# Performance work log

Measured on AMD Instinct MI355X. Metric: run time of the kernel, lower is better.

Reference implementation:

```python
import jax, jax.numpy as jnp
import numpy as np

B, S, D = 2, 2048, 1024
H = 16
HD = D // H  # 64
EPS = 1e-5
ROPE_BASE = 10000.0


def _rope_cos_sin(seq_len, head_dim, dtype):
    # inv_freq over even channel indices, standard rotate-half RoPE
    inv_freq = 1.0 / (ROPE_BASE ** (jnp.arange(0, head_dim, 2, dtype=jnp.float32) / head_dim))
    ang = jnp.arange(seq_len, dtype=jnp.float32)[:, None] * inv_freq[None, :]  # [S, HD/2]
    emb = jnp.concatenate([ang, ang], axis=-1)  # [S, HD]
    return jnp.cos(emb).astype(dtype), jnp.sin(emb).astype(dtype)


def _rotate_half(x):
    x1, x2 = jnp.split(x, 2, axis=-1)
    return jnp.concatenate([-x2, x1], axis=-1)


def setup_inputs() -> dict:
    key = jax.random.key(0)
    ks = jax.random.split(key, 5)
    std = 0.023  # default init_method: normal(mean=0, std=0.023)
    return {
        "hidden_states": jax.random.normal(ks[0], (B, S, D), dtype=jnp.float32),
        "ln_gamma": jnp.ones((D,), dtype=jnp.float32),
        "ln_beta": jnp.zeros((D,), dtype=jnp.float32),
        "qkv_weight": jax.random.normal(ks[1], (3 * D, D), dtype=jnp.float32) * std,
        "qkv_bias": jax.random.normal(ks[2], (3 * D,), dtype=jnp.float32) * std,
        "proj_weight": jax.random.normal(ks[3], (D, D), dtype=jnp.float32) * std,
        "proj_bias": jax.random.normal(ks[4], (D,), dtype=jnp.float32) * std,
    }


def reference(hidden_states, ln_gamma, ln_beta, qkv_weight, qkv_bias, proj_weight, proj_bias):
    b, s, d = hidden_states.shape
    # --- input LayerNorm ---
    mu = jnp.mean(hidden_states, axis=-1, keepdims=True)
    var = jnp.mean(jnp.square(hidden_states - mu), axis=-1, keepdims=True)
    x = (hidden_states - mu) * jax.lax.rsqrt(var + EPS) * ln_gamma + ln_beta

    # --- fused QKV projection (interleaved per-head q,k,v) ---
    qkv = x @ qkv_weight.T + qkv_bias  # [B,S,3D]
    qkv = qkv.reshape(b, s, H, 3, HD)
    q, k, v = qkv[..., 0, :], qkv[..., 1, :], qkv[..., 2, :]  # each [B,S,H,HD]

    # --- RoPE on q and k ---
    cos, sin = _rope_cos_sin(s, HD, q.dtype)  # [S,HD]
    cos = cos[None, :, None, :]
    sin = sin[None, :, None, :]
    q = q * cos + _rotate_half(q) * sin
    k = k * cos + _rotate_half(k) * sin

    # --- causal scaled-dot-product attention ---
    scale = 1.0 / jnp.sqrt(jnp.asarray(HD, dtype=q.dtype))
    scores = jnp.einsum("bqhd,bkhd->bhqk", q, k) * scale  # [B,H,S,S]
    causal = jnp.tril(jnp.ones((s, s), dtype=bool))
    scores = jnp.where(causal[None, None, :, :], scores, jnp.finfo(scores.dtype).min)
    probs = jax.nn.softmax(scores, axis=-1)
    ctx = jnp.einsum("bhqk,bkhd->bqhd", probs, v).reshape(b, s, d)

    # --- output projection ---
    return ctx @ proj_weight.T + proj_bias
```

## Files before the change

kernel.cpp:

```cpp
#include <hip/hip_runtime.h>
#include <math.h>

#define B_  2
#define S_  2048
#define D_  1024
#define H_  16
#define HD_ 64
#define BS_ (B_ * S_)

typedef __bf16 bf16_t;
typedef __bf16 bf16x8 __attribute__((ext_vector_type(8)));
typedef __bf16 bf16x4 __attribute__((ext_vector_type(4)));
typedef float  f32x4  __attribute__((ext_vector_type(4)));
typedef short  s16x4  __attribute__((ext_vector_type(4)));

#define QSCALE 0.18033688011112042f
#define FREQC  0.28782313662425575f

__device__ __forceinline__ void async_ld16(const bf16_t* g, bf16_t* l)
{
    __builtin_amdgcn_global_load_lds(
        (const __attribute__((address_space(1))) void*)g,
        (__attribute__((address_space(3))) void*)l,
        16, 0, 0);
}

__global__ __launch_bounds__(256) void cvt_w(const float* __restrict__ a,
                                             const float* __restrict__ b,
                                             bf16_t* __restrict__ oa,
                                             bf16_t* __restrict__ ob)
{
    int idx = blockIdx.x * 256 + threadIdx.x;
    const int NA = 3 * D_ * D_ / 4;
    if (idx < NA) {
        float4 v = ((const float4*)a)[idx];
        bf16x4 p;
        p[0] = (bf16_t)v.x; p[1] = (bf16_t)v.y; p[2] = (bf16_t)v.z; p[3] = (bf16_t)v.w;
        ((bf16x4*)oa)[idx] = p;
    } else {
        int j = idx - NA;
        float4 v = ((const float4*)b)[j];
        bf16x4 p;
        p[0] = (bf16_t)v.x; p[1] = (bf16_t)v.y; p[2] = (bf16_t)v.z; p[3] = (bf16_t)v.w;
        ((bf16x4*)ob)[j] = p;
    }
}

__global__ __launch_bounds__(256) void ln_kernel(const float* __restrict__ x,
                                                 const float* __restrict__ gamma,
                                                 const float* __restrict__ beta,
                                                 bf16_t* __restrict__ y)
{
    int row = blockIdx.x;
    float4 v = ((const float4*)(x + (size_t)row * D_))[threadIdx.x];
    float sum = v.x + v.y + v.z + v.w;
    float sq  = v.x * v.x + v.y * v.y + v.z * v.z + v.w * v.w;
#pragma unroll
    for (int off = 32; off > 0; off >>= 1) {
        sum += __shfl_down(sum, off);
        sq  += __shfl_down(sq, off);
    }
    __shared__ float s_sum[4], s_sq[4];
    int wave = threadIdx.x >> 6;
    if ((threadIdx.x & 63) == 0) { s_sum[wave] = sum; s_sq[wave] = sq; }
    __syncthreads();
    float tsum = s_sum[0] + s_sum[1] + s_sum[2] + s_sum[3];
    float tsq  = s_sq[0] + s_sq[1] + s_sq[2] + s_sq[3];
    float mean = tsum * (1.0f / D_);
    float var  = tsq * (1.0f / D_) - mean * mean;
    float rstd = rsqrtf(var + 1e-5f);
    float4 g = ((const float4*)gamma)[threadIdx.x];
    float4 b = ((const float4*)beta)[threadIdx.x];
    bf16x4 o;
    o[0] = (bf16_t)((v.x - mean) * rstd * g.x + b.x);
    o[1] = (bf16_t)((v.y - mean) * rstd * g.y + b.y);
    o[2] = (bf16_t)((v.z - mean) * rstd * g.z + b.z);
    o[3] = (bf16_t)((v.w - mean) * rstd * g.w + b.w);
    *(bf16x4*)&y[(size_t)row * D_ + threadIdx.x * 4] = o;
}

template<int MODE>
__global__ __launch_bounds__(256) void gemm_bf16(const bf16_t* __restrict__ A,
                                                 const bf16_t* __restrict__ W,
                                                 const float* __restrict__ bias,
                                                 float* __restrict__ outf,
                                                 bf16_t* __restrict__ qout,
                                                 bf16_t* __restrict__ kout,
                                                 bf16_t* __restrict__ vout,
                                                 int M, int N, int K)
{
    constexpr int SMEM = (MODE == 1) ? 18432 : 16384;
    __shared__ bf16_t smem[SMEM];
    const int bm = blockIdx.y * 128, bn = blockIdx.x * 128;
    const int tid = threadIdx.x;
    const int wave = tid >> 6, lane = tid & 63;
    const int ln16 = lane & 15, quad = lane >> 4;
    const int wr = (wave >> 1) * 64, wc = (wave & 1) * 64;
    const int slot_a = (quad ^ (ln16 & 3)) * 8;

    f32x4 acc[4][4];
#pragma unroll
    for (int i = 0; i < 4; i++)
#pragma unroll
        for (int j = 0; j < 4; j++) acc[i][j] = (f32x4){0.f, 0.f, 0.f, 0.f};

#pragma unroll
    for (int j = 0; j < 2; j++) {
        int e = j * 256 + tid;
        int r = e >> 2, cg = ((e & 3) ^ (r & 3)) * 8;
        async_ld16(&A[(size_t)(bm + r) * K + cg], smem + e * 8);
        async_ld16(&W[(size_t)(bn + r) * K + cg], smem + 4096 + e * 8);
    }
    __syncthreads();

    for (int k0 = 0, it = 0; k0 < K; k0 += 32, it++) {
        const bf16_t* cur = smem + (it & 1) * 8192;
        bf16_t* nxt = smem + ((it & 1) ^ 1) * 8192;
        if (k0 + 32 < K) {
#pragma unroll
            for (int j = 0; j < 2; j++) {
                int e = j * 256 + tid;
                int r = e >> 2, cg = ((e & 3) ^ (r & 3)) * 8;
                async_ld16(&A[(size_t)(bm + r) * K + k0 + 32 + cg], nxt + e * 8);
                async_ld16(&W[(size_t)(bn + r) * K + k0 + 32 + cg], nxt + 4096 + e * 8);
            }
        }

        bf16x8 af[4], bf[4];
#pragma unroll
        for (int mi = 0; mi < 4; mi++)
            af[mi] = *(const bf16x8*)&cur[(wr + mi * 16 + ln16) * 32 + slot_a];
#pragma unroll
        for (int ni = 0; ni < 4; ni++)
            bf[ni] = *(const bf16x8*)&cur[4096 + (wc + ni * 16 + ln16) * 32 + slot_a];
#pragma unroll
        for (int mi = 0; mi < 4; mi++)
#pragma unroll
            for (int ni = 0; ni < 4; ni++)
                acc[mi][ni] = __builtin_amdgcn_mfma_f32_16x16x32_bf16(
                    af[mi], bf[ni], acc[mi][ni], 0, 0, 0);

        __syncthreads();
    }

#pragma unroll
    for (int ni = 0; ni < 4; ni++) {
        float bb = bias[bn + wc + ni * 16 + ln16];
#pragma unroll
        for (int mi = 0; mi < 4; mi++)
#pragma unroll
            for (int r = 0; r < 4; r++) acc[mi][ni][r] += bb;
    }

    if (MODE == 0) {
#pragma unroll
        for (int ni = 0; ni < 4; ni++) {
            int n = bn + wc + ni * 16 + ln16;
#pragma unroll
            for (int mi = 0; mi < 4; mi++)
#pragma unroll
                for (int r = 0; r < 4; r++)
                    outf[(size_t)(bm + wr + mi * 16 + quad * 4 + r) * N + n] = acc[mi][ni][r];
        }
    } else {
        const int n64 = (bn + wc) >> 6;
        const int t = n64 % 3, h = n64 / 3;
        bf16_t* T = smem + wave * (64 * 72);
        if (t == 2) {
#pragma unroll
            for (int mi = 0; mi < 4; mi++) {
#pragma unroll
                for (int ni = 0; ni < 4; ni++) {
                    bf16x4 pk;
#pragma unroll
                    for (int r = 0; r < 4; r++) pk[r] = (bf16_t)acc[mi][ni][r];
                    *(bf16x4*)&T[(ni * 16 + ln16) * 72 + mi * 16 + quad * 4] = pk;
                }
            }
            int m0 = bm + wr;
            int bi = m0 >> 11, s0g = m0 & (S_ - 1);
#pragma unroll
            for (int e = lane; e < 512; e += 64) {
                int hd_l = e >> 3, c8 = (e & 7) << 3;
                *(bf16x8*)&vout[((size_t)(bi * H_ + h) * HD_ + hd_l) * S_ + s0g + c8] =
                    *(const bf16x8*)&T[hd_l * 72 + c8];
            }
        } else {
            float fr0 = __expf(-(float)ln16 * FREQC);
            float fr1 = __expf(-(float)(16 + ln16) * FREQC);
            float sc = (t == 0) ? QSCALE : 1.0f;
#pragma unroll
            for (int mi = 0; mi < 4; mi++) {
#pragma unroll
                for (int r = 0; r < 4; r++) {
                    int m = bm + wr + mi * 16 + quad * 4 + r;
                    float s = (float)(m & (S_ - 1));
                    float sn0, cs0, sn1, cs1;
                    __sincosf(s * fr0, &sn0, &cs0);
                    __sincosf(s * fr1, &sn1, &cs1);
                    int rowo = (mi * 16 + quad * 4 + r) * 72;
                    float x1 = acc[mi][0][r], x2 = acc[mi][2][r];
                    T[rowo + ln16]      = (bf16_t)((x1 * cs0 - x2 * sn0) * sc);
                    T[rowo + 32 + ln16] = (bf16_t)((x2 * cs0 + x1 * sn0) * sc);
                    x1 = acc[mi][1][r]; x2 = acc[mi][3][r];
                    T[rowo + 16 + ln16] = (bf16_t)((x1 * cs1 - x2 * sn1) * sc);
                    T[rowo + 48 + ln16] = (bf16_t)((x2 * cs1 + x1 * sn1) * sc);
                }
            }
            bf16_t* dst = (t == 0) ? qout : kout;
#pragma unroll
            for (int e = lane; e < 512; e += 64) {
                int row_l = e >> 3, c8 = (e & 7) << 3;
                int m = bm + wr + row_l;
                int b = m >> 11, s = m & (S_ - 1);
                *(bf16x8*)&dst[((size_t)(b * H_ + h) * S_ + s) * HD_ + c8] =
                    *(const bf16x8*)&T[row_l * 72 + c8];
            }
        }
    }
}

__global__ __launch_bounds__(256) void attn_p1(const bf16_t* __restrict__ q_buf,
                                               const bf16_t* __restrict__ k_buf,
                                               const bf16_t* __restrict__ v_t,
                                               bf16_t* __restrict__ part_o,
                                               float* __restrict__ part_ml)
{
    __shared__ bf16_t KS[2][4096];
    __shared__ bf16_t VS[2][4096];

    const int x = blockIdx.x, h = blockIdx.y, b = blockIdx.z;
    const int t = (x < 32) ? (31 - x) : (x - 16);
    const int c = (x < 32) ? 0 : 1;
    const int k0c = c * 16;
    const int k1c = min(t, k0c + 15);

    const int tid = threadIdx.x;
    const int wave = tid >> 6, lane = tid & 63;
    const int ln16 = lane & 15, quad = lane >> 4;
    const int w0 = t * 64 + wave * 16;
    const int s7 = ln16 & 7;

    const bf16_t* qb = q_buf + (size_t)(b * H_ + h) * S_ * HD_;
    const bf16_t* kb = k_buf + (size_t)(b * H_ + h) * S_ * HD_;
    const bf16_t* vb = v_t  + (size_t)(b * H_ + h) * HD_ * S_;

    const int e0 = tid, e1 = tid + 256;
    const int r0 = e0 >> 3, c0 = ((e0 & 7) ^ (r0 & 7)) * 8;
    const int r1 = e1 >> 3, c1 = ((e1 & 7) ^ (r1 & 7)) * 8;

    bf16x8 qf[2];
#pragma unroll
    for (int kc = 0; kc < 2; kc++)
        qf[kc] = *(const bf16x8*)&qb[(size_t)(w0 + ln16) * HD_ + kc * 32 + quad * 8];

    f32x4 o[4];
#pragma unroll
    for (int mi = 0; mi < 4; mi++) o[mi] = (f32x4){0.f, 0.f, 0.f, 0.f};
    float m_i = -1e30f, l_i = 0.f;

    {
        bf16x8 ka = *(const bf16x8*)&kb[(size_t)(k0c * 64 + r0) * HD_ + c0];
        bf16x8 kc_ = *(const bf16x8*)&kb[(size_t)(k0c * 64 + r1) * HD_ + c1];
        bf16x8 va = *(const bf16x8*)&vb[(size_t)r0 * S_ + k0c * 64 + c0];
        bf16x8 vc = *(const bf16x8*)&vb[(size_t)r1 * S_ + k0c * 64 + c1];
        int b0 = k0c & 1;
        *(bf16x8*)&KS[b0][e0 * 8] = ka;
        *(bf16x8*)&KS[b0][e1 * 8] = kc_;
        *(bf16x8*)&VS[b0][e0 * 8] = va;
        *(bf16x8*)&VS[b0][e1 * 8] = vc;
    }
    int tp = (k0c + 1 <= k1c) ? (k0c + 1) : k1c;
    bf16x8 kp0 = *(const bf16x8*)&kb[(size_t)(tp * 64 + r0) * HD_ + c0];
    bf16x8 kp1 = *(const bf16x8*)&kb[(size_t)(tp * 64 + r1) * HD_ + c1];
    bf16x8 vp0 = *(const bf16x8*)&vb[(size_t)r0 * S_ + tp * 64 + c0];
    bf16x8 vp1 = *(const bf16x8*)&vb[(size_t)r1 * S_ + tp * 64 + c1];
    __syncthreads();

    for (int kt = k0c; kt <= k1c; kt++) {
        int tn = (kt + 2 <= k1c) ? (kt + 2) : k1c;
        bf16x8 kn0 = *(const bf16x8*)&kb[(size_t)(tn * 64 + r0) * HD_ + c0];
        bf16x8 kn1 = *(const bf16x8*)&kb[(size_t)(tn * 64 + r1) * HD_ + c1];
        bf16x8 vn0 = *(const bf16x8*)&vb[(size_t)r0 * S_ + tn * 64 + c0];
        bf16x8 vn1 = *(const bf16x8*)&vb[(size_t)r1 * S_ + tn * 64 + c1];

        int nb = (kt + 1) & 1;
        *(bf16x8*)&KS[nb][e0 * 8] = kp0;
        *(bf16x8*)&KS[nb][e1 * 8] = kp1;
        *(bf16x8*)&VS[nb][e0 * 8] = vp0;
        *(bf16x8*)&VS[nb][e1 * 8] = vp1;

        const bf16_t* Kc = &KS[kt & 1][0];
        const bf16_t* Vc = &VS[kt & 1][0];

        f32x4 st[4];
#pragma unroll
        for (int cb = 0; cb < 4; cb++) st[cb] = (f32x4){0.f, 0.f, 0.f, 0.f};
#pragma unroll
        for (int kc = 0; kc < 2; kc++)
#pragma unroll
            for (int cb = 0; cb < 4; cb++) {
                bf16x8 kf = *(const bf16x8*)&Kc[(cb * 16 + ln16) * 64 + ((kc * 4 + quad) ^ s7) * 8];
                st[cb] = __builtin_amdgcn_mfma_f32_16x16x32_bf16(kf, qf[kc], st[cb], 0, 0, 0);
            }

        if (kt == t) {
            int q_g = w0 + ln16;
#pragma unroll
            for (int cb = 0; cb < 4; cb++) {
                int key0 = kt * 64 + cb * 16 + quad * 4;
#pragma unroll
                for (int r = 0; r < 4; r++)
                    if (key0 + r > q_g) st[cb][r] = -1e30f;
            }
        }

        float mx = st[0][0];
#pragma unroll
        for (int cb = 0; cb < 4; cb++)
#pragma unroll
            for (int r = 0; r < 4; r++) mx = fmaxf(mx, st[cb][r]);
        mx = fmaxf(mx, __shfl_xor(mx, 16));
        mx = fmaxf(mx, __shfl_xor(mx, 32));
        float mn = fmaxf(m_i, mx);
        float sum = 0.f;
#pragma unroll
        for (int cb = 0; cb < 4; cb++)
#pragma unroll
            for (int r = 0; r < 4; r++) {
                float p = exp2f(st[cb][r] - mn);
                st[cb][r] = p;
                sum += p;
            }
        sum += __shfl_xor(sum, 16);
        sum += __shfl_xor(sum, 32);
        float al = exp2f(m_i - mn);
        l_i = l_i * al + sum;
        m_i = mn;
#pragma unroll
        for (int mi = 0; mi < 4; mi++) {
            o[mi][0] *= al; o[mi][1] *= al; o[mi][2] *= al; o[mi][3] *= al;
        }

        s16x4 pf4[4];
#pragma unroll
        for (int cb = 0; cb < 4; cb++) {
            union { bf16x4 hv; s16x4 sv; } u;
#pragma unroll
            for (int r = 0; r < 4; r++) u.hv[r] = (bf16_t)st[cb][r];
            pf4[cb] = u.sv;
        }

#pragma unroll
        for (int cb = 0; cb < 4; cb++) {
            int slot = ((cb * 2 + (quad >> 1)) ^ s7) * 8 + (quad & 1) * 4;
#pragma unroll
            for (int mi = 0; mi < 4; mi++) {
                union { bf16x4 hv; s16x4 sv; } uv;
                uv.hv = *(const bf16x4*)&Vc[(mi * 16 + ln16) * 64 + slot];
                o[mi] = __builtin_amdgcn_mfma_f32_16x16x16bf16_1k(uv.sv, pf4[cb], o[mi], 0, 0, 0);
            }
        }

        kp0 = kn0; kp1 = kn1; vp0 = vn0; vp1 = vn1;

        __syncthreads();
    }

    const size_t pidx = (((size_t)(b * H_ + h) * 32) + t) * 2 + c;
    bf16_t* po = part_o + pidx * 4096;
    const int q_l = wave * 16 + ln16;
#pragma unroll
    for (int mi = 0; mi < 4; mi++) {
        bf16x4 pk;
#pragma unroll
        for (int r = 0; r < 4; r++) pk[r] = (bf16_t)o[mi][r];
        *(bf16x4*)&po[q_l * 64 + mi * 16 + quad * 4] = pk;
    }
    if (quad == 0) {
        part_ml[pidx * 128 + q_l]      = m_i;
        part_ml[pidx * 128 + 64 + q_l] = l_i;
    }
}

__global__ __launch_bounds__(256) void attn_p2(const bf16_t* __restrict__ part_o,
                                               const float* __restrict__ part_ml,
                                               bf16_t* __restrict__ ctx)
{
    const int t = blockIdx.x, h = blockIdx.y, b = blockIdx.z;
    const int nch = (t >> 4) + 1;
    const size_t pidx = (((size_t)(b * H_ + h) * 32) + t) * 2;
    const int q_l = threadIdx.x >> 2;
    const int hg = (threadIdx.x & 3) * 16;

    float m0 = part_ml[pidx * 128 + q_l];
    float l0 = part_ml[pidx * 128 + 64 + q_l];
    const bf16_t* o0 = part_o + pidx * 4096 + q_l * 64 + hg;

    float w0, w1 = 0.f;
    const bf16_t* o1 = o0;
    if (nch == 2) {
        float m1 = part_ml[(pidx + 1) * 128 + q_l];
        float l1 = part_ml[(pidx + 1) * 128 + 64 + q_l];
        float M = fmaxf(m0, m1);
        float a0 = exp2f(m0 - M), a1 = exp2f(m1 - M);
        float L = a0 * l0 + a1 * l1;
        w0 = a0 / L; w1 = a1 / L;
        o1 = part_o + (pidx + 1) * 4096 + q_l * 64 + hg;
    } else {
        w0 = 1.f / l0;
    }

    bf16x8 a0v = *(const bf16x8*)o0;
    bf16x8 a1v = *(const bf16x8*)(o0 + 8);
    bf16x8 b0v = *(const bf16x8*)o1;
    bf16x8 b1v = *(const bf16x8*)(o1 + 8);
    bf16x8 out0, out1;
#pragma unroll
    for (int i = 0; i < 8; i++) {
        float f0 = (float)a0v[i] * w0 + (float)b0v[i] * w1;
        float f1 = (float)a1v[i] * w0 + (float)b1v[i] * w1;
        out0[i] = (bf16_t)f0;
        out1[i] = (bf16_t)f1;
    }
    bf16_t* dst = &ctx[(size_t)(b * S_ + t * 64 + q_l) * D_ + h * HD_ + hg];
    *(bf16x8*)dst = out0;
    *(bf16x8*)(dst + 8) = out1;
}

extern "C" void kernel_launch(void* const* d_in, const int* in_sizes, int n_in,
                              void* d_out, int out_size, void* d_ws, size_t ws_size,
                              hipStream_t stream)
{
    const float* hidden = (const float*)d_in[0];
    const float* gamma  = (const float*)d_in[1];
    const float* beta   = (const float*)d_in[2];
    const float* qkv_w  = (const float*)d_in[3];
    const float* qkv_b  = (const float*)d_in[4];
    const float* proj_w = (const float*)d_in[5];
    const float* proj_b = (const float*)d_in[6];
    float* out = (float*)d_out;

    char* ws = (char*)d_ws;
    const size_t MB = 1024 * 1024;
    bf16_t* x_ln = (bf16_t*)(ws);
    bf16_t* wq   = (bf16_t*)(ws +  8 * MB);
    bf16_t* wp   = (bf16_t*)(ws + 14 * MB);
    bf16_t* qbf  = (bf16_t*)(ws + 16 * MB);
    bf16_t* kbf  = (bf16_t*)(ws + 24 * MB);
    bf16_t* vtb  = (bf16_t*)(ws + 32 * MB);
    bf16_t* ctx  = (bf16_t*)(ws + 40 * MB);
    bf16_t* po   = (bf16_t*)(ws + 48 * MB);
    float*  pml  = (float*)(ws + 64 * MB);

    cvt_w<<<4096, 256, 0, stream>>>(qkv_w, proj_w, wq, wp);
    ln_kernel<<<BS_, 256, 0, stream>>>(hidden, gamma, beta, x_ln);
    gemm_bf16<1><<<dim3(24, 32), 256, 0, stream>>>(
        x_ln, wq, qkv_b, nullptr, qbf, kbf, vtb, BS_, 3 * D_, D_);
    attn_p1<<<dim3(48, H_, B_), 256, 0, stream>>>(qbf, kbf, vtb, po, pml);
    attn_p2<<<dim3(32, H_, B_), 256, 0, stream>>>(po, pml, ctx);
    gemm_bf16<0><<<dim3(8, 32), 256, 0, stream>>>(
        ctx, wp, proj_b, out, nullptr, nullptr, nullptr, BS_, D_, D_);
}
```

Measured before the change: 211.3 us.

## Fuse LN with weight cast, finer attention KV split, async KV loads, smaller proj tile

Merges the weight-conversion and LayerNorm kernels into a single launch. Attention now splits keys into chunks of up to 8 tiles (up to 4 chunks per query tile, 80 blocks per head) instead of 2 chunks of 16, and the combine kernel merges up to 4 partials. K/V staging switches from register prefetch to direct global-to-LDS async loads. The output projection uses a 64-row M tile to double its block count. Together these aim to cut launch overhead, improve load balance and occupancy, and lower register pressure, at the cost of more partial-result traffic in the combine step.

```diff
diff --git a/kernel.cpp b/kernel.cpp
--- a/kernel.cpp
+++ b/kernel.cpp
@@ -25,32 +25,40 @@
         16, 0, 0);
 }
 
-__global__ __launch_bounds__(256) void cvt_w(const float* __restrict__ a,
-                                             const float* __restrict__ b,
-                                             bf16_t* __restrict__ oa,
-                                             bf16_t* __restrict__ ob)
-{
-    int idx = blockIdx.x * 256 + threadIdx.x;
-    const int NA = 3 * D_ * D_ / 4;
-    if (idx < NA) {
-        float4 v = ((const float4*)a)[idx];
-        bf16x4 p;
-        p[0] = (bf16_t)v.x; p[1] = (bf16_t)v.y; p[2] = (bf16_t)v.z; p[3] = (bf16_t)v.w;
-        ((bf16x4*)oa)[idx] = p;
-    } else {
-        int j = idx - NA;
-        float4 v = ((const float4*)b)[j];
-        bf16x4 p;
-        p[0] = (bf16_t)v.x; p[1] = (bf16_t)v.y; p[2] = (bf16_t)v.z; p[3] = (bf16_t)v.w;
-        ((bf16x4*)ob)[j] = p;
-    }
-}
-
-__global__ __launch_bounds__(256) void ln_kernel(const float* __restrict__ x,
-                                                 const float* __restrict__ gamma,
-                                                 const float* __restrict__ beta,
-                                                 bf16_t* __restrict__ y)
-{
+__device__ __forceinline__ int chunk_base(int t)
+{
+    if (t < 8)  return t;
+    if (t < 16) return 8 + 2 * (t - 8);
+    if (t < 24) return 24 + 3 * (t - 16);
+    return 48 + 4 * (t - 24);
+}
+
+__global__ __launch_bounds__(256) void ln_cvt(const float* __restrict__ x,
+                                              const float* __restrict__ gamma,
+                                              const float* __restrict__ beta,
+                                              bf16_t* __restrict__ y,
+                                              const float* __restrict__ wa,
+                                              const float* __restrict__ wb,
+                                              bf16_t* __restrict__ oa,
+                                              bf16_t* __restrict__ ob)
+{
+    if (blockIdx.x >= BS_) {
+        int idx = (blockIdx.x - BS_) * 256 + threadIdx.x;
+        const int NA = 3 * D_ * D_ / 4;
+        if (idx < NA) {
+            float4 v = ((const float4*)wa)[idx];
+            bf16x4 p;
+            p[0] = (bf16_t)v.x; p[1] = (bf16_t)v.y; p[2] = (bf16_t)v.z; p[3] = (bf16_t)v.w;
+            ((bf16x4*)oa)[idx] = p;
+        } else {
+            int j = idx - NA;
+            float4 v = ((const float4*)wb)[j];
+            bf16x4 p;
+            p[0] = (bf16_t)v.x; p[1] = (bf16_t)v.y; p[2] = (bf16_t)v.z; p[3] = (bf16_t)v.w;
+            ((bf16x4*)ob)[j] = p;
+        }
+        return;
+    }
     int row = blockIdx.x;
     float4 v = ((const float4*)(x + (size_t)row * D_))[threadIdx.x];
     float sum = v.x + v.y + v.z + v.w;
@@ -79,7 +87,7 @@
     *(bf16x4*)&y[(size_t)row * D_ + threadIdx.x * 4] = o;
 }
 
-template<int MODE>
+template<int MODE, int TM>
 __global__ __launch_bounds__(256) void gemm_bf16(const bf16_t* __restrict__ A,
                                                  const bf16_t* __restrict__ W,
                                                  const float* __restrict__ bias,
@@ -89,52 +97,65 @@
                                                  bf16_t* __restrict__ vout,
                                                  int M, int N, int K)
 {
-    constexpr int SMEM = (MODE == 1) ? 18432 : 16384;
+    constexpr int ASZ = TM * 32;
+    constexpr int BUF = ASZ + 4096;
+    constexpr int SMEM = (MODE == 1) ? 18432 : 2 * BUF;
+    constexpr int MI = (TM == 128) ? 4 : 2;
     __shared__ bf16_t smem[SMEM];
-    const int bm = blockIdx.y * 128, bn = blockIdx.x * 128;
+    const int bm = blockIdx.y * TM, bn = blockIdx.x * 128;
     const int tid = threadIdx.x;
     const int wave = tid >> 6, lane = tid & 63;
     const int ln16 = lane & 15, quad = lane >> 4;
-    const int wr = (wave >> 1) * 64, wc = (wave & 1) * 64;
+    const int wr = (wave >> 1) * (TM / 2), wc = (wave & 1) * 64;
     const int slot_a = (quad ^ (ln16 & 3)) * 8;
 
-    f32x4 acc[4][4];
-#pragma unroll
-    for (int i = 0; i < 4; i++)
+    f32x4 acc[MI][4];
+#pragma unroll
+    for (int i = 0; i < MI; i++)
 #pragma unroll
         for (int j = 0; j < 4; j++) acc[i][j] = (f32x4){0.f, 0.f, 0.f, 0.f};
 
+#pragma unroll
+    for (int j = 0; j < TM / 64; j++) {
+        int e = j * 256 + tid;
+        int r = e >> 2, cg = ((e & 3) ^ (r & 3)) * 8;
+        async_ld16(&A[(size_t)(bm + r) * K + cg], smem + e * 8);
+    }
 #pragma unroll
     for (int j = 0; j < 2; j++) {
         int e = j * 256 + tid;
         int r = e >> 2, cg = ((e & 3) ^ (r & 3)) * 8;
-        async_ld16(&A[(size_t)(bm + r) * K + cg], smem + e * 8);
-        async_ld16(&W[(size_t)(bn + r) * K + cg], smem + 4096 + e * 8);
+        async_ld16(&W[(size_t)(bn + r) * K + cg], smem + ASZ + e * 8);
     }
     __syncthreads();
 
     for (int k0 = 0, it = 0; k0 < K; k0 += 32, it++) {
-        const bf16_t* cur = smem + (it & 1) * 8192;
-        bf16_t* nxt = smem + ((it & 1) ^ 1) * 8192;
+        const bf16_t* cur = smem + (it & 1) * BUF;
+        bf16_t* nxt = smem + ((it & 1) ^ 1) * BUF;
         if (k0 + 32 < K) {
+#pragma unroll
+            for (int j = 0; j < TM / 64; j++) {
+                int e = j * 256 + tid;
+                int r = e >> 2, cg = ((e & 3) ^ (r & 3)) * 8;
+                async_ld16(&A[(size_t)(bm + r) * K + k0 + 32 + cg], nxt + e * 8);
+            }
 #pragma unroll
             for (int j = 0; j < 2; j++) {
                 int e = j * 256 + tid;
                 int r = e >> 2, cg = ((e & 3) ^ (r & 3)) * 8;
-                async_ld16(&A[(size_t)(bm + r) * K + k0 + 32 + cg], nxt + e * 8);
-                async_ld16(&W[(size_t)(bn + r) * K + k0 + 32 + cg], nxt + 4096 + e * 8);
-            }
-        }
-
-        bf16x8 af[4], bf[4];
-#pragma unroll
-        for (int mi = 0; mi < 4; mi++)
+                async_ld16(&W[(size_t)(bn + r) * K + k0 + 32 + cg], nxt + ASZ + e * 8);
+            }
+        }
+
+        bf16x8 af[MI], bf[4];
+#pragma unroll
+        for (int mi = 0; mi < MI; mi++)
             af[mi] = *(const bf16x8*)&cur[(wr + mi * 16 + ln16) * 32 + slot_a];
 #pragma unroll
         for (int ni = 0; ni < 4; ni++)
-            bf[ni] = *(const bf16x8*)&cur[4096 + (wc + ni * 16 + ln16) * 32 + slot_a];
-#pragma unroll
-        for (int mi = 0; mi < 4; mi++)
+            bf[ni] = *(const bf16x8*)&cur[ASZ + (wc + ni * 16 + ln16) * 32 + slot_a];
+#pragma unroll
+        for (int mi = 0; mi < MI; mi++)
 #pragma unroll
             for (int ni = 0; ni < 4; ni++)
                 acc[mi][ni] = __builtin_amdgcn_mfma_f32_16x16x32_bf16(
@@ -147,7 +168,7 @@
     for (int ni = 0; ni < 4; ni++) {
         float bb = bias[bn + wc + ni * 16 + ln16];
 #pragma unroll
-        for (int mi = 0; mi < 4; mi++)
+        for (int mi = 0; mi < MI; mi++)
 #pragma unroll
             for (int r = 0; r < 4; r++) acc[mi][ni][r] += bb;
     }
@@ -157,7 +178,7 @@
         for (int ni = 0; ni < 4; ni++) {
             int n = bn + wc + ni * 16 + ln16;
 #pragma unroll
-            for (int mi = 0; mi < 4; mi++)
+            for (int mi = 0; mi < MI; mi++)
 #pragma unroll
                 for (int r = 0; r < 4; r++)
                     outf[(size_t)(bm + wr + mi * 16 + quad * 4 + r) * N + n] = acc[mi][ni][r];
@@ -229,11 +250,15 @@
     __shared__ bf16_t KS[2][4096];
     __shared__ bf16_t VS[2][4096];
 
-    const int x = blockIdx.x, h = blockIdx.y, b = blockIdx.z;
-    const int t = (x < 32) ? (31 - x) : (x - 16);
-    const int c = (x < 32) ? 0 : 1;
-    const int k0c = c * 16;
-    const int k1c = min(t, k0c + 15);
+    const int h = blockIdx.y, b = blockIdx.z;
+    const int xx = 79 - blockIdx.x;
+    int t, c;
+    if (xx < 8)       { t = xx;                c = 0; }
+    else if (xx < 24) { int y = xx - 8;  t = 8 + (y >> 1);  c = y & 1; }
+    else if (xx < 48) { int y = xx - 24; int q = y / 3; t = 16 + q; c = y - 3 * q; }
+    else              { int y = xx - 48; t = 24 + (y >> 2); c = y & 3; }
+    const int k0c = c * 8;
+    const int k1c = min(t, k0c + 7);
 
     const int tid = threadIdx.x;
     const int wave = tid >> 6, lane = tid & 63;
@@ -259,77 +284,62 @@
     for (int mi = 0; mi < 4; mi++) o[mi] = (f32x4){0.f, 0.f, 0.f, 0.f};
     float m_i = -1e30f, l_i = 0.f;
 
-    {
-        bf16x8 ka = *(const bf16x8*)&kb[(size_t)(k0c * 64 + r0) * HD_ + c0];
-        bf16x8 kc_ = *(const bf16x8*)&kb[(size_t)(k0c * 64 + r1) * HD_ + c1];
-        bf16x8 va = *(const bf16x8*)&vb[(size_t)r0 * S_ + k0c * 64 + c0];
-        bf16x8 vc = *(const bf16x8*)&vb[(size_t)r1 * S_ + k0c * 64 + c1];
-        int b0 = k0c & 1;
-        *(bf16x8*)&KS[b0][e0 * 8] = ka;
-        *(bf16x8*)&KS[b0][e1 * 8] = kc_;
-        *(bf16x8*)&VS[b0][e0 * 8] = va;
-        *(bf16x8*)&VS[b0][e1 * 8] = vc;
-    }
-    int tp = (k0c + 1 <= k1c) ? (k0c + 1) : k1c;
-    bf16x8 kp0 = *(const bf16x8*)&kb[(size_t)(tp * 64 + r0) * HD_ + c0];
-    bf16x8 kp1 = *(const bf16x8*)&kb[(size_t)(tp * 64 + r1) * HD_ + c1];
-    bf16x8 vp0 = *(const bf16x8*)&vb[(size_t)r0 * S_ + tp * 64 + c0];
-    bf16x8 vp1 = *(const bf16x8*)&vb[(size_t)r1 * S_ + tp * 64 + c1];
+    async_ld16(&kb[(size_t)(k0c * 64 + r0) * HD_ + c0], &KS[0][e0 * 8]);
+    async_ld16(&kb[(size_t)(k0c * 64 + r1) * HD_ + c1], &KS[0][e1 * 8]);
+    async_ld16(&vb[(size_t)r0 * S_ + k0c * 64 + c0], &VS[0][e0 * 8]);
+    async_ld16(&vb[(size_t)r1 * S_ + k0c * 64 + c1], &VS[0][e1 * 8]);
     __syncthreads();
 
     for (int kt = k0c; kt <= k1c; kt++) {
-        int tn = (kt + 2 <= k1c) ? (kt + 2) : k1c;
-        bf16x8 kn0 = *(const bf16x8*)&kb[(size_t)(tn * 64 + r0) * HD_ + c0];
-        bf16x8 kn1 = *(const bf16x8*)&kb[(size_t)(tn * 64 + r1) * HD_ + c1];
-        bf16x8 vn0 = *(const bf16x8*)&vb[(size_t)r0 * S_ + tn * 64 + c0];
-        bf16x8 vn1 = *(const bf16x8*)&vb[(size_t)r1 * S_ + tn * 64 + c1];
-
-        int nb = (kt + 1) & 1;
-        *(bf16x8*)&KS[nb][e0 * 8] = kp0;
-        *(bf16x8*)&KS[nb][e1 * 8] = kp1;
-        *(bf16x8*)&VS[nb][e0 * 8] = vp0;
-        *(bf16x8*)&VS[nb][e1 * 8] = vp1;
-
-        const bf16_t* Kc = &KS[kt & 1][0];
-        const bf16_t* Vc = &VS[kt & 1][0];
+        const int cb = (kt - k0c) & 1;
+        if (kt < k1c) {
+            const int nb = cb ^ 1, kn = kt + 1;
+            async_ld16(&kb[(size_t)(kn * 64 + r0) * HD_ + c0], &KS[nb][e0 * 8]);
+            async_ld16(&kb[(size_t)(kn * 64 + r1) * HD_ + c1], &KS[nb][e1 * 8]);
+            async_ld16(&vb[(size_t)r0 * S_ + kn * 64 + c0], &VS[nb][e0 * 8]);
+            async_ld16(&vb[(size_t)r1 * S_ + kn * 64 + c1], &VS[nb][e1 * 8]);
+        }
+
+        const bf16_t* Kc = &KS[cb][0];
+        const bf16_t* Vc = &VS[cb][0];
 
         f32x4 st[4];
 #pragma unroll
-        for (int cb = 0; cb < 4; cb++) st[cb] = (f32x4){0.f, 0.f, 0.f, 0.f};
+        for (int cbx = 0; cbx < 4; cbx++) st[cbx] = (f32x4){0.f, 0.f, 0.f, 0.f};
 #pragma unroll
         for (int kc = 0; kc < 2; kc++)
 #pragma unroll
-            for (int cb = 0; cb < 4; cb++) {
-                bf16x8 kf = *(const bf16x8*)&Kc[(cb * 16 + ln16) * 64 + ((kc * 4 + quad) ^ s7) * 8];
-                st[cb] = __builtin_amdgcn_mfma_f32_16x16x32_bf16(kf, qf[kc], st[cb], 0, 0, 0);
+            for (int cbx = 0; cbx < 4; cbx++) {
+                bf16x8 kf = *(const bf16x8*)&Kc[(cbx * 16 + ln16) * 64 + ((kc * 4 + quad) ^ s7) * 8];
+                st[cbx] = __builtin_amdgcn_mfma_f32_16x16x32_bf16(kf, qf[kc], st[cbx], 0, 0, 0);
             }
 
         if (kt == t) {
             int q_g = w0 + ln16;
 #pragma unroll
-            for (int cb = 0; cb < 4; cb++) {
-                int key0 = kt * 64 + cb * 16 + quad * 4;
+            for (int cbx = 0; cbx < 4; cbx++) {
+                int key0 = kt * 64 + cbx * 16 + quad * 4;
 #pragma unroll
                 for (int r = 0; r < 4; r++)
-                    if (key0 + r > q_g) st[cb][r] = -1e30f;
+                    if (key0 + r > q_g) st[cbx][r] = -1e30f;
             }
         }
 
         float mx = st[0][0];
 #pragma unroll
-        for (int cb = 0; cb < 4; cb++)
-#pragma unroll
-            for (int r = 0; r < 4; r++) mx = fmaxf(mx, st[cb][r]);
+        for (int cbx = 0; cbx < 4; cbx++)
+#pragma unroll
+            for (int r = 0; r < 4; r++) mx = fmaxf(mx, st[cbx][r]);
         mx = fmaxf(mx, __shfl_xor(mx, 16));
         mx = fmaxf(mx, __shfl_xor(mx, 32));
         float mn = fmaxf(m_i, mx);
         float sum = 0.f;
 #pragma unroll
-        for (int cb = 0; cb < 4; cb++)
+        for (int cbx = 0; cbx < 4; cbx++)
 #pragma unroll
             for (int r = 0; r < 4; r++) {
-                float p = exp2f(st[cb][r] - mn);
-                st[cb][r] = p;
+                float p = exp2f(st[cbx][r] - mn);
+                st[cbx][r] = p;
                 sum += p;
             }
         sum += __shfl_xor(sum, 16);
@@ -344,30 +354,28 @@
 
         s16x4 pf4[4];
 #pragma unroll
-        for (int cb = 0; cb < 4; cb++) {
+        for (int cbx = 0; cbx < 4; cbx++) {
             union { bf16x4 hv; s16x4 sv; } u;
 #pragma unroll
-            for (int r = 0; r < 4; r++) u.hv[r] = (bf16_t)st[cb][r];
-            pf4[cb] = u.sv;
-        }
-
-#pragma unroll
-        for (int cb = 0; cb < 4; cb++) {
-            int slot = ((cb * 2 + (quad >> 1)) ^ s7) * 8 + (quad & 1) * 4;
+            for (int r = 0; r < 4; r++) u.hv[r] = (bf16_t)st[cbx][r];
+            pf4[cbx] = u.sv;
+        }
+
+#pragma unroll
+        for (int cbx = 0; cbx < 4; cbx++) {
+            int slot = ((cbx * 2 + (quad >> 1)) ^ s7) * 8 + (quad & 1) * 4;
 #pragma unroll
             for (int mi = 0; mi < 4; mi++) {
                 union { bf16x4 hv; s16x4 sv; } uv;
                 uv.hv = *(const bf16x4*)&Vc[(mi * 16 + ln16) * 64 + slot];
-                o[mi] = __builtin_amdgcn_mfma_f32_16x16x16bf16_1k(uv.sv, pf4[cb], o[mi], 0, 0, 0);
-            }
-        }
-
-        kp0 = kn0; kp1 = kn1; vp0 = vn0; vp1 = vn1;
+                o[mi] = __builtin_amdgcn_mfma_f32_16x16x16bf16_1k(uv.sv, pf4[cbx], o[mi], 0, 0, 0);
+            }
+        }
 
         __syncthreads();
     }
 
-    const size_t pidx = (((size_t)(b * H_ + h) * 32) + t) * 2 + c;
+    const size_t pidx = (size_t)(b * H_ + h) * 80 + chunk_base(t) + c;
     bf16_t* po = part_o + pidx * 4096;
     const int q_l = wave * 16 + ln16;
 #pragma unroll
@@ -388,41 +396,47 @@
                                                bf16_t* __restrict__ ctx)
 {
     const int t = blockIdx.x, h = blockIdx.y, b = blockIdx.z;
-    const int nch = (t >> 4) + 1;
-    const size_t pidx = (((size_t)(b * H_ + h) * 32) + t) * 2;
+    const int nch = (t >> 3) + 1;
+    const size_t p0 = (size_t)(b * H_ + h) * 80 + chunk_base(t);
     const int q_l = threadIdx.x >> 2;
     const int hg = (threadIdx.x & 3) * 16;
 
-    float m0 = part_ml[pidx * 128 + q_l];
-    float l0 = part_ml[pidx * 128 + 64 + q_l];
-    const bf16_t* o0 = part_o + pidx * 4096 + q_l * 64 + hg;
-
-    float w0, w1 = 0.f;
-    const bf16_t* o1 = o0;
-    if (nch == 2) {
-        float m1 = part_ml[(pidx + 1) * 128 + q_l];
-        float l1 = part_ml[(pidx + 1) * 128 + 64 + q_l];
-        float M = fmaxf(m0, m1);
-        float a0 = exp2f(m0 - M), a1 = exp2f(m1 - M);
-        float L = a0 * l0 + a1 * l1;
-        w0 = a0 / L; w1 = a1 / L;
-        o1 = part_o + (pidx + 1) * 4096 + q_l * 64 + hg;
-    } else {
-        w0 = 1.f / l0;
-    }
-
-    bf16x8 a0v = *(const bf16x8*)o0;
-    bf16x8 a1v = *(const bf16x8*)(o0 + 8);
-    bf16x8 b0v = *(const bf16x8*)o1;
-    bf16x8 b1v = *(const bf16x8*)(o1 + 8);
+    float m[4], l[4];
+    float M = -1e30f;
+#pragma unroll
+    for (int i = 0; i < 4; i++) {
+        if (i < nch) {
+            m[i] = part_ml[(p0 + i) * 128 + q_l];
+            l[i] = part_ml[(p0 + i) * 128 + 64 + q_l];
+            M = fmaxf(M, m[i]);
+        }
+    }
+    float w[4], L = 0.f;
+#pragma unroll
+    for (int i = 0; i < 4; i++) {
+        if (i < nch) { w[i] = exp2f(m[i] - M); L += w[i] * l[i]; }
+        else w[i] = 0.f;
+    }
+    float invL = 1.0f / L;
+
+    float f0[8] = {0,0,0,0,0,0,0,0}, f1[8] = {0,0,0,0,0,0,0,0};
+#pragma unroll
+    for (int i = 0; i < 4; i++) {
+        if (i < nch) {
+            const bf16_t* oi = part_o + (p0 + i) * 4096 + q_l * 64 + hg;
+            bf16x8 v0 = *(const bf16x8*)oi;
+            bf16x8 v1 = *(const bf16x8*)(oi + 8);
+            float wi = w[i] * invL;
+#pragma unroll
+            for (int j = 0; j < 8; j++) {
+                f0[j] += (float)v0[j] * wi;
+                f1[j] += (float)v1[j] * wi;
+            }
+        }
+    }
     bf16x8 out0, out1;
 #pragma unroll
-    for (int i = 0; i < 8; i++) {
-        float f0 = (float)a0v[i] * w0 + (float)b0v[i] * w1;
-        float f1 = (float)a1v[i] * w0 + (float)b1v[i] * w1;
-        out0[i] = (bf16_t)f0;
-        out1[i] = (bf16_t)f1;
-    }
+    for (int j = 0; j < 8; j++) { out0[j] = (bf16_t)f0[j]; out1[j] = (bf16_t)f1[j]; }
     bf16_t* dst = &ctx[(size_t)(b * S_ + t * 64 + q_l) * D_ + h * HD_ + hg];
     *(bf16x8*)dst = out0;
     *(bf16x8*)(dst + 8) = out1;
@@ -451,14 +465,14 @@
     bf16_t* vtb  = (bf16_t*)(ws + 32 * MB);
     bf16_t* ctx  = (bf16_t*)(ws + 40 * MB);
     bf16_t* po   = (bf16_t*)(ws + 48 * MB);
-    float*  pml  = (float*)(ws + 64 * MB);
-
-    cvt_w<<<4096, 256, 0, stream>>>(qkv_w, proj_w, wq, wp);
-    ln_kernel<<<BS_, 256, 0, stream>>>(hidden, gamma, beta, x_ln);
-    gemm_bf16<1><<<dim3(24, 32), 256, 0, stream>>>(
+    float*  pml  = (float*)(ws + 68 * MB);
+
+    ln_cvt<<<BS_ + 4096, 256, 0, stream>>>(hidden, gamma, beta, x_ln,
+                                           qkv_w, proj_w, wq, wp);
+    gemm_bf16<1, 128><<<dim3(24, 32), 256, 0, stream>>>(
         x_ln, wq, qkv_b, nullptr, qbf, kbf, vtb, BS_, 3 * D_, D_);
-    attn_p1<<<dim3(48, H_, B_), 256, 0, stream>>>(qbf, kbf, vtb, po, pml);
+    attn_p1<<<dim3(80, H_, B_), 256, 0, stream>>>(qbf, kbf, vtb, po, pml);
     attn_p2<<<dim3(32, H_, B_), 256, 0, stream>>>(po, pml, ctx);
-    gemm_bf16<0><<<dim3(8, 32), 256, 0, stream>>>(
+    gemm_bf16<0, 64><<<dim3(8, 64), 256, 0, stream>>>(
         ctx, wp, proj_b, out, nullptr, nullptr, nullptr, BS_, D_, D_);
 }
```

Result: faster. 199.3 us (-5.7%).
